# Optimization experiments

Hardware: AMD Instinct MI355X
Metric: run time of the kernel (lower is better)

## Reference

```python
import jax, jax.numpy as jnp
import numpy as np

NUM_HEADS = 16

def setup_inputs() -> dict:
    key = jax.random.key(0)
    x = jax.random.normal(key, (4, 2048, 1024), dtype=jnp.float32)
    return {"x": x}

def reference(x) -> jnp.ndarray:
    B, T, D = x.shape
    H = NUM_HEADS
    hd = D // H
    xh = x.reshape(B, T, H, hd)                      # [B,T,H,hd]
    x_centered = xh - jnp.mean(xh, axis=1, keepdims=True)
    # mean-centered QK^T: [B,H,T,T]
    corr = jnp.einsum('bthd,bThd->bhtT', x_centered, x_centered)
    corr = jax.nn.softmax(corr, axis=-1)
    # weighted sum with UNcentered values
    out = jnp.einsum('bhtT,bThd->bthd', corr, xh)    # [B,T,H,hd]
    return out.reshape(B, T, D)
```

## Files before the change

### kernel.cpp

```cpp
#include <hip/hip_runtime.h>
#include <stdint.h>

#define B_   4
#define T_   2048
#define H_   16
#define HD_  64
#define D_   1024
#define QB   128
#define KB   64
#define NSTEP (T_ / KB)
#define NROUND (NSTEP / 2)
#define L2E   1.44269504088896f
#define SQL2E 1.20112240878645f
#define THR2  15.5f
#define M2INIT 28.8539f
#define SKIPTHR (-24.5f)

typedef __attribute__((ext_vector_type(4)))  float    f32x4;
typedef __attribute__((ext_vector_type(16))) float    f32x16;
typedef __attribute__((ext_vector_type(8)))  _Float16 f16x8;
typedef __attribute__((ext_vector_type(2)))  __fp16   h16x2;

__device__ __forceinline__ f32x4 mfma16(f16x8 a, f16x8 b, f32x4 c) {
  return __builtin_amdgcn_mfma_f32_16x16x32_f16(a, b, c, 0, 0, 0);
}
__device__ __forceinline__ f32x16 mfma32(f16x8 a, f16x8 b, f32x16 c) {
  return __builtin_amdgcn_mfma_f32_32x32x16_f16(a, b, c, 0, 0, 0);
}
__device__ __forceinline__ f32x16 zero16() {
  f32x16 z;
  #pragma unroll
  for (int i = 0; i < 16; ++i) z[i] = 0.f;
  return z;
}
__device__ __forceinline__ float fexp2(float x) {
#if __has_builtin(__builtin_amdgcn_exp2f)
  return __builtin_amdgcn_exp2f(x);
#else
  return exp2f(x);
#endif
}
__device__ __forceinline__ uint32_t pkrtz_u(float a, float b) {
  h16x2 r = __builtin_amdgcn_cvt_pkrtz(a, b);
  return __builtin_bit_cast(uint32_t, r);
}
__device__ __forceinline__ float fdot2_u(uint32_t a, h16x2 ones, float c) {
  return __builtin_amdgcn_fdot2(__builtin_bit_cast(h16x2, a), ones, c, false);
}
__device__ __forceinline__ void pl32swap(uint32_t& a, uint32_t& b) {
  asm volatile("v_permlane32_swap_b32 %0, %1" : "+v"(a), "+v"(b));
}
__device__ __forceinline__ f16x8 mk_frag(uint32_t u0, uint32_t u1,
                                         uint32_t u2, uint32_t u3) {
  union { uint32_t u[4]; f16x8 v; } x;
  x.u[0] = u0; x.u[1] = u1; x.u[2] = u2; x.u[3] = u3;
  return x.v;
}
__device__ __forceinline__ void gld16(const void* g, void* l) {
  __builtin_amdgcn_global_load_lds(
      (const __attribute__((address_space(1))) uint32_t*)g,
      (__attribute__((address_space(3))) uint32_t*)l, 16, 0, 0);
}

__global__ __launch_bounds__(256)
void colmean_kernel(const float* __restrict__ x, float* __restrict__ mu) {
  const int b   = blockIdx.x >> 6;
  const int c0  = (blockIdx.x & 63) << 4;
  const int col = threadIdx.x & 15;
  const int rg  = threadIdx.x >> 4;
  const float* p = x + ((size_t)(b * T_ + rg * 128)) * D_ + c0 + col;
  float s = 0.f;
  #pragma unroll 8
  for (int r = 0; r < 128; ++r) s += p[(size_t)r * D_];
  __shared__ float red[16][17];
  red[rg][col] = s;
  __syncthreads();
  if (rg == 0) {
    float t = 0.f;
    #pragma unroll
    for (int i = 0; i < 16; ++i) t += red[i][col];
    mu[b * D_ + c0 + col] = t * (1.f / (float)T_);
  }
}

__global__ __launch_bounds__(256)
void cvt2_kernel(const float* __restrict__ x, const float* __restrict__ mu,
                 _Float16* __restrict__ KT, _Float16* __restrict__ VT) {
  const int unit = blockIdx.x * 4 + (threadIdx.x >> 6);
  const int bh   = unit >> 5;
  const int tile = unit & 31;
  const int b    = bh >> 4;
  const int h    = bh & 15;
  const int lane = threadIdx.x & 63;
  const int t    = tile * 64 + lane;

  const float* xr  = x  + ((size_t)(b * T_ + t)) * D_ + h * HD_;
  const float* mur = mu + b * D_ + h * HD_;

  _Float16 cfV[64];
  _Float16 cfK[64];
  #pragma unroll
  for (int u = 0; u < 16; ++u) {
    float4 f = *(const float4*)(xr + u * 4);
    float4 m = *(const float4*)(mur + u * 4);
    float c0 = f.x - m.x, c1 = f.y - m.y, c2 = f.z - m.z, c3 = f.w - m.w;
    cfV[u*4+0] = (_Float16)c0; cfK[u*4+0] = (_Float16)(c0 * SQL2E);
    cfV[u*4+1] = (_Float16)c1; cfK[u*4+1] = (_Float16)(c1 * SQL2E);
    cfV[u*4+2] = (_Float16)c2; cfK[u*4+2] = (_Float16)(c2 * SQL2E);
    cfV[u*4+3] = (_Float16)c3; cfK[u*4+3] = (_Float16)(c3 * SQL2E);
  }
  _Float16* kt = KT + ((size_t)(bh * 32 + tile)) * 4096;
  #pragma unroll
  for (int g = 0; g < 8; ++g)
    *(f16x8*)&kt[g * 512 + lane * 8] = *(const f16x8*)&cfK[g * 8];
  _Float16* vt = VT + ((size_t)(bh * 32 + tile)) * 4096 + (lane >> 3) * 512 + (lane & 7);
  #pragma unroll
  for (int d = 0; d < 64; ++d) vt[d * 8] = cfV[d];
}

__global__ __launch_bounds__(256, 4)
void attn12_kernel(const _Float16* __restrict__ KT,
                   const _Float16* __restrict__ VT,
                   const float* __restrict__ mu,
                   float* __restrict__ out) {
  __shared__ __align__(16) _Float16 Kb[4][4096];

  const int tid  = threadIdx.x;
  const int lane = tid & 63;
  const int wv   = tid >> 6;
  const int c    = lane & 31;
  const int hp   = lane >> 5;

  const int bid = blockIdx.x;
  const int wid = (bid & 7) * 128 + (bid >> 3);
  const int qb  = wid & 15;
  const int bh  = wid >> 4;
  const int b   = bh >> 4;
  const int h   = bh & 15;

  const int q0w = qb * QB + wv * 32;
  const int start = 2 * qb;

  f16x8 qf[4];
  {
    const _Float16* qt = KT + ((size_t)(bh * 32 + (q0w >> 6))) * 4096;
    const int qrow = ((wv & 1) * 32) + c;
    #pragma unroll
    for (int s = 0; s < 4; ++s)
      qf[s] = *(const f16x8*)&qt[(2 * s + hp) * 512 + qrow * 8];
  }

  const char* kbase = (const char*)KT + ((size_t)(bh * 32)) * 8192 + wv * 2048 + lane * 16;
  const int fb = hp * 512 + c * 8;

  const _Float16* vfrag = VT + ((size_t)(bh * 32)) * 4096 + fb;

  f32x16 acc0 = zero16(), acc1 = zero16();
  f32x16 C1 = zero16();
  #pragma unroll
  for (int i = 0; i < 16; ++i) C1[i] = -M2INIT;
  float lrun = 0.f;
  h16x2 one2; one2[0] = (__fp16)1.0f; one2[1] = (__fp16)1.0f;

  {
    const char* s0p = kbase + (size_t)start * 8192;
    gld16(s0p,        &Kb[0][wv * 1024]);
    gld16(s0p + 1024, &Kb[0][wv * 1024 + 512]);
    const char* s1p = kbase + (size_t)((start + 1) & 31) * 8192;
    gld16(s1p,        &Kb[1][wv * 1024]);
    gld16(s1p + 1024, &Kb[1][wv * 1024 + 512]);
  }
  __syncthreads();

  for (int r = 0; r < NROUND; ++r) {
    const int rd = (r & 1) << 1;
    const int wr = rd ^ 2;

    if (r + 1 < NROUND) {
      const char* p0 = kbase + (size_t)((start + 2*r + 2) & 31) * 8192;
      gld16(p0,        &Kb[wr][wv * 1024]);
      gld16(p0 + 1024, &Kb[wr][wv * 1024 + 512]);
      const char* p1 = kbase + (size_t)((start + 2*r + 3) & 31) * 8192;
      gld16(p1,        &Kb[wr + 1][wv * 1024]);
      gld16(p1 + 1024, &Kb[wr + 1][wv * 1024 + 512]);
    }

    #pragma unroll
    for (int sub = 0; sub < 2; ++sub) {
      const _Float16* Kp = &Kb[rd + sub][fb];
      const _Float16* Vp = vfrag + (size_t)((start + 2*r + sub) & 31) * 4096;

      #pragma unroll
      for (int kt = 0; kt < 2; ++kt) {
        f32x16 st;
        __builtin_amdgcn_s_setprio(1);
        st = mfma32(*(const f16x8*)&Kp[0 * 1024 + kt * 256], qf[0], C1);
        st = mfma32(*(const f16x8*)&Kp[1 * 1024 + kt * 256], qf[1], st);
        st = mfma32(*(const f16x8*)&Kp[2 * 1024 + kt * 256], qf[2], st);
        st = mfma32(*(const f16x8*)&Kp[3 * 1024 + kt * 256], qf[3], st);
        __builtin_amdgcn_s_setprio(0);

        float m0 = fmaxf(fmaxf(st[0],  st[1]),  st[2]);
        float m1 = fmaxf(fmaxf(st[3],  st[4]),  st[5]);
        float m2 = fmaxf(fmaxf(st[6],  st[7]),  st[8]);
        float m3 = fmaxf(fmaxf(st[9],  st[10]), st[11]);
        float m4 = fmaxf(fmaxf(st[12], st[13]), st[14]);
        float pm = fmaxf(fmaxf(fmaxf(m0, m1), fmaxf(m2, m3)), fmaxf(m4, st[15]));

        if (__all(pm <= SKIPTHR)) continue;

        const float pmw = fmaxf(pm, __shfl_xor(pm, 32));
        if (!__all(pm <= THR2)) {
          const float dm  = fmaxf(pmw, 0.f);
          const float al  = fexp2(-dm);
          lrun *= al;
          #pragma unroll
          for (int ii = 0; ii < 16; ++ii) { C1[ii] -= dm; st[ii] -= dm; }
          #pragma unroll
          for (int rr = 0; rr < 16; ++rr) {
            const int row = (rr & 3) + 8 * (rr >> 2) + 4 * hp;
            const float a = __shfl(al, row);
            acc0[rr] *= a; acc1[rr] *= a;
          }
        }

        f16x8 v0a = *(const f16x8*)&Vp[(2*kt    ) * 1024      ];
        f16x8 v1a = *(const f16x8*)&Vp[(2*kt + 1) * 1024      ];
        f16x8 v0b = *(const f16x8*)&Vp[(2*kt    ) * 1024 + 256];
        f16x8 v1b = *(const f16x8*)&Vp[(2*kt + 1) * 1024 + 256];

        f16x8 paL, paH;
        float rsA = 0.f, rsB = 0.f;
        #pragma unroll
        for (int v = 0; v < 2; ++v) {
          uint32_t A0 = pkrtz_u(fexp2(st[8*v+0]), fexp2(st[8*v+1]));
          uint32_t A1 = pkrtz_u(fexp2(st[8*v+2]), fexp2(st[8*v+3]));
          uint32_t B0 = pkrtz_u(fexp2(st[8*v+4]), fexp2(st[8*v+5]));
          uint32_t B1 = pkrtz_u(fexp2(st[8*v+6]), fexp2(st[8*v+7]));
          rsA = fdot2_u(A0, one2, rsA); rsA = fdot2_u(A1, one2, rsA);
          rsB = fdot2_u(B0, one2, rsB); rsB = fdot2_u(B1, one2, rsB);
          pl32swap(A0, B0);
          pl32swap(A1, B1);
          if (v == 0) paL = mk_frag(A0, A1, B0, B1);
          else        paH = mk_frag(A0, A1, B0, B1);
        }
        lrun += rsA + rsB;

        __builtin_amdgcn_s_setprio(1);
        acc0 = mfma32(paL, v0a, acc0);
        acc0 = mfma32(paH, v1a, acc0);
        acc1 = mfma32(paL, v0b, acc1);
        acc1 = mfma32(paH, v1b, acc1);
        __builtin_amdgcn_s_setprio(0);
      }
    }

    if (r + 1 < NROUND) __syncthreads();
  }

  const float ltot = lrun + __shfl_xor(lrun, 32);
  const float linv = 1.0f / ltot;
  const float mv0 = mu[b * D_ + h * HD_ + c];
  const float mv1 = mu[b * D_ + h * HD_ + 32 + c];
  #pragma unroll
  for (int r = 0; r < 16; ++r) {
    const int row = (r & 3) + 8 * (r >> 2) + 4 * hp;
    const float lr = __shfl(linv, row);
    const int q = q0w + row;
    float* orow = out + (size_t)(b * T_ + q) * D_ + h * HD_;
    orow[c]      = acc0[r] * lr + mv0;
    orow[32 + c] = acc1[r] * lr + mv1;
  }
}

__global__ __launch_bounds__(256)
void attn_fb_kernel(const float* __restrict__ x, const float* __restrict__ mu,
                    float* __restrict__ out) {
  __shared__ __align__(16) _Float16 Kt[64 * 64];
  __shared__ __align__(16) _Float16 Vt[64 * 64];
  __shared__ __align__(16) _Float16 Pl[4][2][16 * 64];

  const int tid  = threadIdx.x;
  const int lane = tid & 63;
  const int wv   = tid >> 6;
  const int j    = lane & 15;
  const int g    = lane >> 4;

  const int qb = blockIdx.x & 15;
  const int bh = blockIdx.x >> 4;
  const int b  = bh >> 4;
  const int h  = bh & 15;

  const float* xb  = x  + (size_t)b * T_ * D_;
  const float* muh = mu + b * D_ + h * HD_;

  f16x8 qf[2][2];
  const int q0 = qb * 128 + wv * 32;
  #pragma unroll
  for (int qt = 0; qt < 2; ++qt) {
    const float* qrow = xb + (size_t)(q0 + qt * 16 + j) * D_ + h * HD_;
    #pragma unroll
    for (int ks = 0; ks < 2; ++ks) {
      const int d0 = ks * 32 + g * 8;
      float4 a  = *(const float4*)(qrow + d0);
      float4 cc = *(const float4*)(qrow + d0 + 4);
      float4 m0 = *(const float4*)(muh + d0);
      float4 m1 = *(const float4*)(muh + d0 + 4);
      f16x8 f;
      f[0] = (_Float16)(a.x - m0.x); f[1] = (_Float16)(a.y - m0.y);
      f[2] = (_Float16)(a.z - m0.z); f[3] = (_Float16)(a.w - m0.w);
      f[4] = (_Float16)(cc.x - m1.x); f[5] = (_Float16)(cc.y - m1.y);
      f[6] = (_Float16)(cc.z - m1.z); f[7] = (_Float16)(cc.w - m1.w);
      qf[qt][ks] = f;
    }
  }

  const int kd0 = (tid & 7) * 8;
  const float4 kmu0 = *(const float4*)(muh + kd0);
  const float4 kmu1 = *(const float4*)(muh + kd0 + 4);
  const int vd2 = (tid & 31) * 2;
  const int vkc = tid >> 5;

  f32x4 acc[2][4];
  float mrun[2][4], lrun[2][4];
  #pragma unroll
  for (int qt = 0; qt < 2; ++qt) {
    #pragma unroll
    for (int n = 0; n < 4; ++n) acc[qt][n] = f32x4{0.f, 0.f, 0.f, 0.f};
    #pragma unroll
    for (int r = 0; r < 4; ++r) { mrun[qt][r] = -1e30f; lrun[qt][r] = 0.f; }
  }

  const int swj = (j & 7) << 3;

  for (int step = 0; step < NSTEP; ++step) {
    const size_t krow0 = (size_t)(step * KB) * D_ + h * HD_;
    __syncthreads();

    #pragma unroll
    for (int cc2 = 0; cc2 < 2; ++cc2) {
      const int kk = (tid >> 3) + cc2 * 32;
      const float* src = xb + krow0 + (size_t)kk * D_ + kd0;
      float4 a = *(const float4*)src;
      float4 cc = *(const float4*)(src + 4);
      f16x8 f;
      f[0] = (_Float16)(a.x - kmu0.x); f[1] = (_Float16)(a.y - kmu0.y);
      f[2] = (_Float16)(a.z - kmu0.z); f[3] = (_Float16)(a.w - kmu0.w);
      f[4] = (_Float16)(cc.x - kmu1.x); f[5] = (_Float16)(cc.y - kmu1.y);
      f[6] = (_Float16)(cc.z - kmu1.z); f[7] = (_Float16)(cc.w - kmu1.w);
      *(f16x8*)&Kt[kk * 64 + (kd0 ^ ((kk & 7) << 3))] = f;
    }
    {
      float2 t[8];
      #pragma unroll
      for (int e = 0; e < 8; ++e)
        t[e] = *(const float2*)(xb + krow0 + (size_t)(vkc * 8 + e) * D_ + vd2);
      f16x8 f0, f1;
      #pragma unroll
      for (int e = 0; e < 8; ++e) { f0[e] = (_Float16)t[e].x; f1[e] = (_Float16)t[e].y; }
      *(f16x8*)&Vt[(vd2    ) * 64 + ((vkc * 8) ^ (((vd2    ) & 7) << 3))] = f0;
      *(f16x8*)&Vt[(vd2 + 1) * 64 + ((vkc * 8) ^ (((vd2 + 1) & 7) << 3))] = f1;
    }
    __syncthreads();

    f32x4 s[2][4];
    #pragma unroll
    for (int n = 0; n < 4; ++n) {
      const int rb = (n * 16 + j) * 64;
      f16x8 kb0 = *(const f16x8*)&Kt[rb + (((     g * 8)) ^ swj)];
      f16x8 kb1 = *(const f16x8*)&Kt[rb + (((32 + g * 8)) ^ swj)];
      #pragma unroll
      for (int qt = 0; qt < 2; ++qt) {
        f32x4 z = f32x4{0.f, 0.f, 0.f, 0.f};
        z = mfma16(qf[qt][0], kb0, z);
        s[qt][n] = mfma16(qf[qt][1], kb1, z);
      }
    }

    #pragma unroll
    for (int qt = 0; qt < 2; ++qt) {
      float al[4];
      #pragma unroll
      for (int r = 0; r < 4; ++r) {
        float v = fmaxf(fmaxf(s[qt][0][r], s[qt][1][r]),
                        fmaxf(s[qt][2][r], s[qt][3][r]));
        v = fmaxf(v, __shfl_xor(v, 1, 16));
        v = fmaxf(v, __shfl_xor(v, 2, 16));
        v = fmaxf(v, __shfl_xor(v, 4, 16));
        v = fmaxf(v, __shfl_xor(v, 8, 16));
        const float mn = fmaxf(mrun[qt][r], v);
        al[r] = exp2f((mrun[qt][r] - mn) * L2E);
        mrun[qt][r] = mn;
        float p0 = exp2f((s[qt][0][r] - mn) * L2E);
        float p1 = exp2f((s[qt][1][r] - mn) * L2E);
        float p2 = exp2f((s[qt][2][r] - mn) * L2E);
        float p3 = exp2f((s[qt][3][r] - mn) * L2E);
        float rs = (p0 + p1) + (p2 + p3);
        rs += __shfl_xor(rs, 1, 16);
        rs += __shfl_xor(rs, 2, 16);
        rs += __shfl_xor(rs, 4, 16);
        rs += __shfl_xor(rs, 8, 16);
        lrun[qt][r] = lrun[qt][r] * al[r] + rs;
        const int q   = g * 4 + r;
        const int qsw = (q & 7) << 3;
        _Float16* prow = &Pl[wv][qt][q * 64];
        prow[(     j) ^ qsw] = (_Float16)p0;
        prow[(16 + j) ^ qsw] = (_Float16)p1;
        prow[(32 + j) ^ qsw] = (_Float16)p2;
        prow[(48 + j) ^ qsw] = (_Float16)p3;
      }
      #pragma unroll
      for (int n = 0; n < 4; ++n) {
        acc[qt][n][0] *= al[0]; acc[qt][n][1] *= al[1];
        acc[qt][n][2] *= al[2]; acc[qt][n][3] *= al[3];
      }
    }

    asm volatile("s_waitcnt lgkmcnt(0)" ::: "memory");

    f16x8 pa[2][2];
    #pragma unroll
    for (int qt = 0; qt < 2; ++qt) {
      const _Float16* Pw = &Pl[wv][qt][0];
      pa[qt][0] = *(const f16x8*)&Pw[j * 64 + (((     g * 8)) ^ swj)];
      pa[qt][1] = *(const f16x8*)&Pw[j * 64 + (((32 + g * 8)) ^ swj)];
    }
    #pragma unroll
    for (int n = 0; n < 4; ++n) {
      const int rb = (n * 16 + j) * 64;
      f16x8 v0 = *(const f16x8*)&Vt[rb + (((     g * 8)) ^ swj)];
      f16x8 v1 = *(const f16x8*)&Vt[rb + (((32 + g * 8)) ^ swj)];
      #pragma unroll
      for (int qt = 0; qt < 2; ++qt) {
        acc[qt][n] = mfma16(pa[qt][0], v0, acc[qt][n]);
        acc[qt][n] = mfma16(pa[qt][1], v1, acc[qt][n]);
      }
    }
  }

  #pragma unroll
  for (int qt = 0; qt < 2; ++qt) {
    float inv[4];
    #pragma unroll
    for (int r = 0; r < 4; ++r) inv[r] = 1.0f / lrun[qt][r];
    #pragma unroll
    for (int n = 0; n < 4; ++n) {
      #pragma unroll
      for (int r = 0; r < 4; ++r) {
        const int q = q0 + qt * 16 + g * 4 + r;
        out[(size_t)(b * T_ + q) * D_ + h * HD_ + n * 16 + j] =
            acc[qt][n][r] * inv[r];
      }
    }
  }
}

extern "C" void kernel_launch(void* const* d_in, const int* in_sizes, int n_in,
                              void* d_out, int out_size, void* d_ws, size_t ws_size,
                              hipStream_t stream) {
  (void)in_sizes; (void)n_in; (void)out_size;
  const float* x  = (const float*)d_in[0];
  float* outp     = (float*)d_out;

  const size_t MU_BYTES  = (size_t)B_ * D_ * sizeof(float);
  const size_t C16_BYTES = (size_t)B_ * T_ * D_ * 2;

  float* mu = (float*)d_ws;
  hipLaunchKernelGGL(colmean_kernel, dim3(B_ * 64), dim3(256), 0, stream, x, mu);

  if (ws_size >= MU_BYTES + 2 * C16_BYTES) {
    _Float16* KT = (_Float16*)((char*)d_ws + MU_BYTES);
    _Float16* VT = (_Float16*)((char*)d_ws + MU_BYTES + C16_BYTES);
    hipLaunchKernelGGL(cvt2_kernel, dim3(512), dim3(256), 0, stream, x, mu, KT, VT);
    hipLaunchKernelGGL(attn12_kernel, dim3((T_ / QB) * B_ * H_), dim3(256), 0, stream,
                       KT, VT, mu, outp);
  } else {
    hipLaunchKernelGGL(attn_fb_kernel, dim3((T_ / 128) * B_ * H_), dim3(256), 0, stream,
                       x, mu, outp);
  }
}
```

Baseline: 82.74 us.

## Replace double-round K staging with 4-slot ring buffer and partial vmcnt waits

The K tile loading changes from a two-round double buffer (two 64-key tiles per round, full __syncthreads per round) to a four-slot ring that prefetches three tiles ahead. It synchronises each step with an explicit s_waitcnt vmcnt(N) followed by s_barrier, so only the oldest tile's loads must complete. The aim is to keep more global-to-LDS loads in flight and avoid draining all outstanding loads at every barrier. The cost is one barrier per 64-key step instead of one per 128, and the hand-written vmcnt counts assume no other vector memory operations are pending, such as the V global loads. If that assumption fails, the waits become stricter than intended.

New measurement: 83.65 us. No clear change (+1.1%).

```diff
diff --git a/kernel.cpp b/kernel.cpp
--- a/kernel.cpp
+++ b/kernel.cpp
@@ -9,7 +9,6 @@
 #define QB   128
 #define KB   64
 #define NSTEP (T_ / KB)
-#define NROUND (NSTEP / 2)
 #define L2E   1.44269504088896f
 #define SQL2E 1.20112240878645f
 #define THR2  15.5f
@@ -119,7 +118,7 @@
 }
 
 __global__ __launch_bounds__(256, 4)
-void attn12_kernel(const _Float16* __restrict__ KT,
+void attn13_kernel(const _Float16* __restrict__ KT,
                    const _Float16* __restrict__ VT,
                    const float* __restrict__ mu,
                    float* __restrict__ out) {
@@ -162,100 +161,98 @@
   float lrun = 0.f;
   h16x2 one2; one2[0] = (__fp16)1.0f; one2[1] = (__fp16)1.0f;
 
-  {
-    const char* s0p = kbase + (size_t)start * 8192;
-    gld16(s0p,        &Kb[0][wv * 1024]);
-    gld16(s0p + 1024, &Kb[0][wv * 1024 + 512]);
-    const char* s1p = kbase + (size_t)((start + 1) & 31) * 8192;
-    gld16(s1p,        &Kb[1][wv * 1024]);
-    gld16(s1p + 1024, &Kb[1][wv * 1024 + 512]);
-  }
-  __syncthreads();
-
-  for (int r = 0; r < NROUND; ++r) {
-    const int rd = (r & 1) << 1;
-    const int wr = rd ^ 2;
-
-    if (r + 1 < NROUND) {
-      const char* p0 = kbase + (size_t)((start + 2*r + 2) & 31) * 8192;
-      gld16(p0,        &Kb[wr][wv * 1024]);
-      gld16(p0 + 1024, &Kb[wr][wv * 1024 + 512]);
-      const char* p1 = kbase + (size_t)((start + 2*r + 3) & 31) * 8192;
-      gld16(p1,        &Kb[wr + 1][wv * 1024]);
-      gld16(p1 + 1024, &Kb[wr + 1][wv * 1024 + 512]);
-    }
-
-    #pragma unroll
-    for (int sub = 0; sub < 2; ++sub) {
-      const _Float16* Kp = &Kb[rd + sub][fb];
-      const _Float16* Vp = vfrag + (size_t)((start + 2*r + sub) & 31) * 4096;
-
-      #pragma unroll
-      for (int kt = 0; kt < 2; ++kt) {
-        f32x16 st;
-        __builtin_amdgcn_s_setprio(1);
-        st = mfma32(*(const f16x8*)&Kp[0 * 1024 + kt * 256], qf[0], C1);
-        st = mfma32(*(const f16x8*)&Kp[1 * 1024 + kt * 256], qf[1], st);
-        st = mfma32(*(const f16x8*)&Kp[2 * 1024 + kt * 256], qf[2], st);
-        st = mfma32(*(const f16x8*)&Kp[3 * 1024 + kt * 256], qf[3], st);
-        __builtin_amdgcn_s_setprio(0);
-
-        float m0 = fmaxf(fmaxf(st[0],  st[1]),  st[2]);
-        float m1 = fmaxf(fmaxf(st[3],  st[4]),  st[5]);
-        float m2 = fmaxf(fmaxf(st[6],  st[7]),  st[8]);
-        float m3 = fmaxf(fmaxf(st[9],  st[10]), st[11]);
-        float m4 = fmaxf(fmaxf(st[12], st[13]), st[14]);
-        float pm = fmaxf(fmaxf(fmaxf(m0, m1), fmaxf(m2, m3)), fmaxf(m4, st[15]));
-
-        if (__all(pm <= SKIPTHR)) continue;
-
-        const float pmw = fmaxf(pm, __shfl_xor(pm, 32));
-        if (!__all(pm <= THR2)) {
-          const float dm  = fmaxf(pmw, 0.f);
-          const float al  = fexp2(-dm);
-          lrun *= al;
-          #pragma unroll
-          for (int ii = 0; ii < 16; ++ii) { C1[ii] -= dm; st[ii] -= dm; }
-          #pragma unroll
-          for (int rr = 0; rr < 16; ++rr) {
-            const int row = (rr & 3) + 8 * (rr >> 2) + 4 * hp;
-            const float a = __shfl(al, row);
-            acc0[rr] *= a; acc1[rr] *= a;
-          }
+  #pragma unroll
+  for (int t = 0; t < 3; ++t) {
+    const char* sp = kbase + (size_t)((start + t) & 31) * 8192;
+    gld16(sp,        &Kb[t][wv * 1024]);
+    gld16(sp + 1024, &Kb[t][wv * 1024 + 512]);
+  }
+  __builtin_amdgcn_sched_barrier(0);
+  asm volatile("s_waitcnt vmcnt(4)" ::: "memory");
+  __builtin_amdgcn_s_barrier();
+  __builtin_amdgcn_sched_barrier(0);
+
+  for (int i = 0; i < NSTEP; ++i) {
+    if (i + 3 < NSTEP) {
+      const char* sp = kbase + (size_t)((start + i + 3) & 31) * 8192;
+      gld16(sp,        &Kb[(i + 3) & 3][wv * 1024]);
+      gld16(sp + 1024, &Kb[(i + 3) & 3][wv * 1024 + 512]);
+    }
+    const _Float16* Kp = &Kb[i & 3][fb];
+    const _Float16* Vp = vfrag + (size_t)((start + i) & 31) * 4096;
+
+    #pragma unroll
+    for (int kt = 0; kt < 2; ++kt) {
+      f32x16 st;
+      __builtin_amdgcn_s_setprio(1);
+      st = mfma32(*(const f16x8*)&Kp[0 * 1024 + kt * 256], qf[0], C1);
+      st = mfma32(*(const f16x8*)&Kp[1 * 1024 + kt * 256], qf[1], st);
+      st = mfma32(*(const f16x8*)&Kp[2 * 1024 + kt * 256], qf[2], st);
+      st = mfma32(*(const f16x8*)&Kp[3 * 1024 + kt * 256], qf[3], st);
+      __builtin_amdgcn_s_setprio(0);
+
+      float n0 = fmaxf(fmaxf(st[0],  st[1]),  st[2]);
+      float n1 = fmaxf(fmaxf(st[3],  st[4]),  st[5]);
+      float n2 = fmaxf(fmaxf(st[6],  st[7]),  st[8]);
+      float n3 = fmaxf(fmaxf(st[9],  st[10]), st[11]);
+      float n4 = fmaxf(fmaxf(st[12], st[13]), st[14]);
+      float pm = fmaxf(fmaxf(fmaxf(n0, n1), fmaxf(n2, n3)), fmaxf(n4, st[15]));
+
+      if (__all(pm <= SKIPTHR)) continue;
+
+      const float pmw = fmaxf(pm, __shfl_xor(pm, 32));
+      if (!__all(pm <= THR2)) {
+        const float dm  = fmaxf(pmw, 0.f);
+        const float al  = fexp2(-dm);
+        lrun *= al;
+        #pragma unroll
+        for (int ii = 0; ii < 16; ++ii) { C1[ii] -= dm; st[ii] -= dm; }
+        #pragma unroll
+        for (int rr = 0; rr < 16; ++rr) {
+          const int row = (rr & 3) + 8 * (rr >> 2) + 4 * hp;
+          const float a = __shfl(al, row);
+          acc0[rr] *= a; acc1[rr] *= a;
         }
-
-        f16x8 v0a = *(const f16x8*)&Vp[(2*kt    ) * 1024      ];
-        f16x8 v1a = *(const f16x8*)&Vp[(2*kt + 1) * 1024      ];
-        f16x8 v0b = *(const f16x8*)&Vp[(2*kt    ) * 1024 + 256];
-        f16x8 v1b = *(const f16x8*)&Vp[(2*kt + 1) * 1024 + 256];
-
-        f16x8 paL, paH;
-        float rsA = 0.f, rsB = 0.f;
-        #pragma unroll
-        for (int v = 0; v < 2; ++v) {
-          uint32_t A0 = pkrtz_u(fexp2(st[8*v+0]), fexp2(st[8*v+1]));
-          uint32_t A1 = pkrtz_u(fexp2(st[8*v+2]), fexp2(st[8*v+3]));
-          uint32_t B0 = pkrtz_u(fexp2(st[8*v+4]), fexp2(st[8*v+5]));
-          uint32_t B1 = pkrtz_u(fexp2(st[8*v+6]), fexp2(st[8*v+7]));
-          rsA = fdot2_u(A0, one2, rsA); rsA = fdot2_u(A1, one2, rsA);
-          rsB = fdot2_u(B0, one2, rsB); rsB = fdot2_u(B1, one2, rsB);
-          pl32swap(A0, B0);
-          pl32swap(A1, B1);
-          if (v == 0) paL = mk_frag(A0, A1, B0, B1);
-          else        paH = mk_frag(A0, A1, B0, B1);
-        }
-        lrun += rsA + rsB;
-
-        __builtin_amdgcn_s_setprio(1);
-        acc0 = mfma32(paL, v0a, acc0);
-        acc0 = mfma32(paH, v1a, acc0);
-        acc1 = mfma32(paL, v0b, acc1);
-        acc1 = mfma32(paH, v1b, acc1);
-        __builtin_amdgcn_s_setprio(0);
-      }
-    }
-
-    if (r + 1 < NROUND) __syncthreads();
+      }
+
+      f16x8 v0a = *(const f16x8*)&Vp[(2*kt    ) * 1024      ];
+      f16x8 v1a = *(const f16x8*)&Vp[(2*kt + 1) * 1024      ];
+      f16x8 v0b = *(const f16x8*)&Vp[(2*kt    ) * 1024 + 256];
+      f16x8 v1b = *(const f16x8*)&Vp[(2*kt + 1) * 1024 + 256];
+
+      f16x8 paL, paH;
+      float rsA = 0.f, rsB = 0.f;
+      #pragma unroll
+      for (int v = 0; v < 2; ++v) {
+        uint32_t A0 = pkrtz_u(fexp2(st[8*v+0]), fexp2(st[8*v+1]));
+        uint32_t A1 = pkrtz_u(fexp2(st[8*v+2]), fexp2(st[8*v+3]));
+        uint32_t B0 = pkrtz_u(fexp2(st[8*v+4]), fexp2(st[8*v+5]));
+        uint32_t B1 = pkrtz_u(fexp2(st[8*v+6]), fexp2(st[8*v+7]));
+        rsA = fdot2_u(A0, one2, rsA); rsA = fdot2_u(A1, one2, rsA);
+        rsB = fdot2_u(B0, one2, rsB); rsB = fdot2_u(B1, one2, rsB);
+        pl32swap(A0, B0);
+        pl32swap(A1, B1);
+        if (v == 0) paL = mk_frag(A0, A1, B0, B1);
+        else        paH = mk_frag(A0, A1, B0, B1);
+      }
+      lrun += rsA + rsB;
+
+      __builtin_amdgcn_s_setprio(1);
+      acc0 = mfma32(paL, v0a, acc0);
+      acc0 = mfma32(paH, v1a, acc0);
+      acc1 = mfma32(paL, v0b, acc1);
+      acc1 = mfma32(paH, v1b, acc1);
+      __builtin_amdgcn_s_setprio(0);
+    }
+
+    if (i + 1 < NSTEP) {
+      __builtin_amdgcn_sched_barrier(0);
+      if      (i + 3 < NSTEP) asm volatile("s_waitcnt vmcnt(4)" ::: "memory");
+      else if (i + 2 < NSTEP) asm volatile("s_waitcnt vmcnt(2)" ::: "memory");
+      else                    asm volatile("s_waitcnt vmcnt(0)" ::: "memory");
+      __builtin_amdgcn_s_barrier();
+      __builtin_amdgcn_sched_barrier(0);
+    }
   }
 
   const float ltot = lrun + __shfl_xor(lrun, 32);
@@ -472,7 +469,7 @@
     _Float16* KT = (_Float16*)((char*)d_ws + MU_BYTES);
     _Float16* VT = (_Float16*)((char*)d_ws + MU_BYTES + C16_BYTES);
     hipLaunchKernelGGL(cvt2_kernel, dim3(512), dim3(256), 0, stream, x, mu, KT, VT);
-    hipLaunchKernelGGL(attn12_kernel, dim3((T_ / QB) * B_ * H_), dim3(256), 0, stream,
+    hipLaunchKernelGGL(attn13_kernel, dim3((T_ / QB) * B_ * H_), dim3(256), 0, stream,
                        KT, VT, mu, outp);
   } else {
     hipLaunchKernelGGL(attn_fb_kernel, dim3((T_ / 128) * B_ * H_), dim3(256), 0, stream,
```
